# Kernel tuning notes

Measured on AMD Instinct MI355X. Metric: run time of the kernel, lower is better.

Reference implementation:

```python
import jax, jax.numpy as jnp
import numpy as np

ALPHA = 1.0
NUM_SEGMENTS = 50000  # number of structures (segments)


def setup_inputs() -> dict:
    key = jax.random.key(0)
    k1, k2, k3 = jax.random.split(key, 3)
    n, d = 1000000, 128
    prop = jax.random.normal(k1, (1, n, d), dtype=jnp.float32)
    weights = jax.random.uniform(k2, (1, n), dtype=jnp.float32)
    index = jnp.sort(jax.random.randint(k3, (1, n), 0, NUM_SEGMENTS, dtype=jnp.int32))
    return {"prop": prop, "weights": weights, "index": index}


def reference(prop, weights, index):
    # result_s = sum_{i in segment s} w_i^alpha * prop_i / sum_{i in s} w_i^alpha
    expo_w = weights ** ALPHA                      # [1, n]
    idx = index.reshape(-1)                        # [n]
    weighted = prop * expo_w[:, :, None]           # [1, n, d]
    prop_sum = jax.ops.segment_sum(weighted[0], idx, num_segments=NUM_SEGMENTS)[None]   # [1, S, d]
    weight_sum = jax.ops.segment_sum(expo_w[0], idx, num_segments=NUM_SEGMENTS)[None]   # [1, S]
    return prop_sum / weight_sum[:, :, None]
```

## Files before the change

### kernel.cpp

```cpp
#include <hip/hip_runtime.h>
#include <hip/hip_bf16.h>

#define NUM_SEGMENTS 50000

__global__ void build_starts(const int* __restrict__ idx,
                             int* __restrict__ starts,
                             int n, int S) {
    int i = blockIdx.x * blockDim.x + threadIdx.x;
    if (i >= n) return;
    int cur = idx[i];
    if (i == 0) {
        for (int s = 0; s <= cur; ++s) starts[s] = 0;
    } else {
        int prev = idx[i - 1];
        for (int s = prev + 1; s <= cur; ++s) starts[s] = i;
    }
    if (i == n - 1) {
        for (int s = cur + 1; s <= S; ++s) starts[s] = n;
    }
}

__global__ void __launch_bounds__(128)
seg_weighted_avg(const float* __restrict__ prop,
                 const float* __restrict__ w,
                 const int*   __restrict__ starts,
                 float*       __restrict__ out,
                 int d) {
    const int s     = blockIdx.x;
    const int start = starts[s];
    const int end   = starts[s + 1];
    const int t     = threadIdx.x;

    const float* p = prop + (size_t)start * d + t;
    float acc  = 0.0f;
    float wsum = 0.0f;

    int i = start;
    const int d2 = d * 2, d3 = d * 3, d4 = d * 4;
    for (; i + 4 <= end; i += 4) {
        float w0 = w[i], w1 = w[i + 1], w2 = w[i + 2], w3 = w[i + 3];
        float p0 = p[0], p1 = p[d], p2 = p[d2], p3 = p[d3];
        p += d4;
        acc  = fmaf(w0, p0, acc);
        acc  = fmaf(w1, p1, acc);
        acc  = fmaf(w2, p2, acc);
        acc  = fmaf(w3, p3, acc);
        wsum += (w0 + w1) + (w2 + w3);
    }
    for (; i < end; ++i) {
        float wi = w[i];
        wsum += wi;
        acc  = fmaf(wi, p[0], acc);
        p += d;
    }

    out[(size_t)s * d + t] = acc / wsum;
}

extern "C" void kernel_launch(void* const* d_in, const int* in_sizes, int n_in,
                              void* d_out, int out_size, void* d_ws, size_t ws_size,
                              hipStream_t stream) {
    const float* prop = (const float*)d_in[0];
    const float* w    = (const float*)d_in[1];
    const int*   idx  = (const int*)d_in[2];
    float* out        = (float*)d_out;

    const int n = in_sizes[1];
    const int d = in_sizes[0] / in_sizes[1];
    const int S = NUM_SEGMENTS;

    int* starts = (int*)d_ws;

    build_starts<<<(n + 255) / 256, 256, 0, stream>>>(idx, starts, n, S);
    seg_weighted_avg<<<S, d, 0, stream>>>(prop, w, starts, out, d);
}
```

Before: 106.8 us.

## Vectorize d=128 segment reduction with float4 loads and row-group split

Adds a specialized kernel for d=128 in which each thread loads float4 columns and the four wavefront-sized groups process interleaved rows of a segment. The partial sums are reduced through shared memory before the divide. This is meant to cut load instruction count and increase memory-level parallelism per segment, which averages about 20 rows. In exchange it adds a shared-memory reduction and a barrier per block, and only 32 threads write the output.

```diff
diff --git a/kernel.cpp b/kernel.cpp
--- a/kernel.cpp
+++ b/kernel.cpp
@@ -21,39 +21,80 @@
 }
 
 __global__ void __launch_bounds__(128)
-seg_weighted_avg(const float* __restrict__ prop,
-                 const float* __restrict__ w,
-                 const int*   __restrict__ starts,
-                 float*       __restrict__ out,
-                 int d) {
+seg_weighted_avg_d128(const float4* __restrict__ prop4,
+                      const float*  __restrict__ w,
+                      const int*    __restrict__ starts,
+                      float4*       __restrict__ out4) {
+    const int s     = blockIdx.x;
+    const int start = starts[s];
+    const int nrows = starts[s + 1] - start;
+
+    const int t    = threadIdx.x;
+    const int col4 = t & 31;
+    const int rg   = t >> 5;
+
+    const float4* p = prop4 + (size_t)(start + rg) * 32 + col4;
+    const float*  wp = w + start;
+
+    float4 acc = make_float4(0.f, 0.f, 0.f, 0.f);
+    float wsum = 0.0f;
+
+    int r = rg;
+    for (; r + 4 < nrows; r += 8) {
+        float  w0 = wp[r],        w1 = wp[r + 4];
+        float4 p0 = p[0],         p1 = p[128];
+        p += 256;
+        acc.x = fmaf(w0, p0.x, acc.x); acc.y = fmaf(w0, p0.y, acc.y);
+        acc.z = fmaf(w0, p0.z, acc.z); acc.w = fmaf(w0, p0.w, acc.w);
+        acc.x = fmaf(w1, p1.x, acc.x); acc.y = fmaf(w1, p1.y, acc.y);
+        acc.z = fmaf(w1, p1.z, acc.z); acc.w = fmaf(w1, p1.w, acc.w);
+        wsum += w0 + w1;
+    }
+    for (; r < nrows; r += 4) {
+        float  w0 = wp[r];
+        float4 p0 = p[0];
+        p += 128;
+        acc.x = fmaf(w0, p0.x, acc.x); acc.y = fmaf(w0, p0.y, acc.y);
+        acc.z = fmaf(w0, p0.z, acc.z); acc.w = fmaf(w0, p0.w, acc.w);
+        wsum += w0;
+    }
+
+    __shared__ float4 lacc[128];
+    __shared__ float  lw[128];
+    lacc[t] = acc;
+    lw[t]   = wsum;
+    __syncthreads();
+
+    if (t < 32) {
+        float4 a0 = lacc[t], a1 = lacc[t + 32], a2 = lacc[t + 64], a3 = lacc[t + 96];
+        float ws = (lw[t] + lw[t + 32]) + (lw[t + 64] + lw[t + 96]);
+        float4 res;
+        res.x = ((a0.x + a1.x) + (a2.x + a3.x)) / ws;
+        res.y = ((a0.y + a1.y) + (a2.y + a3.y)) / ws;
+        res.z = ((a0.z + a1.z) + (a2.z + a3.z)) / ws;
+        res.w = ((a0.w + a1.w) + (a2.w + a3.w)) / ws;
+        out4[(size_t)s * 32 + t] = res;
+    }
+}
+
+__global__ void __launch_bounds__(128)
+seg_weighted_avg_generic(const float* __restrict__ prop,
+                         const float* __restrict__ w,
+                         const int*   __restrict__ starts,
+                         float*       __restrict__ out,
+                         int d) {
     const int s     = blockIdx.x;
     const int start = starts[s];
     const int end   = starts[s + 1];
     const int t     = threadIdx.x;
-
-    const float* p = prop + (size_t)start * d + t;
-    float acc  = 0.0f;
-    float wsum = 0.0f;
-
-    int i = start;
-    const int d2 = d * 2, d3 = d * 3, d4 = d * 4;
-    for (; i + 4 <= end; i += 4) {
-        float w0 = w[i], w1 = w[i + 1], w2 = w[i + 2], w3 = w[i + 3];
-        float p0 = p[0], p1 = p[d], p2 = p[d2], p3 = p[d3];
-        p += d4;
-        acc  = fmaf(w0, p0, acc);
-        acc  = fmaf(w1, p1, acc);
-        acc  = fmaf(w2, p2, acc);
-        acc  = fmaf(w3, p3, acc);
-        wsum += (w0 + w1) + (w2 + w3);
-    }
-    for (; i < end; ++i) {
+    const float* p  = prop + (size_t)start * d + t;
+    float acc = 0.f, wsum = 0.f;
+    for (int i = start; i < end; ++i) {
         float wi = w[i];
         wsum += wi;
-        acc  = fmaf(wi, p[0], acc);
+        acc = fmaf(wi, p[0], acc);
         p += d;
     }
-
     out[(size_t)s * d + t] = acc / wsum;
 }
 
@@ -72,5 +113,11 @@
     int* starts = (int*)d_ws;
 
     build_starts<<<(n + 255) / 256, 256, 0, stream>>>(idx, starts, n, S);
-    seg_weighted_avg<<<S, d, 0, stream>>>(prop, w, starts, out, d);
+
+    if (d == 128) {
+        seg_weighted_avg_d128<<<S, 128, 0, stream>>>(
+            (const float4*)prop, w, starts, (float4*)out);
+    } else {
+        seg_weighted_avg_generic<<<S, d, 0, stream>>>(prop, w, starts, out, d);
+    }
 }
```

New measurement: 106.5 us. Within noise of the previous version (-0.3%).
